# Kernel optimization log

Hardware: AMD Instinct MI355X
Metric: run time of the kernel (lower is better)

Reference implementation:

```python
import jax, jax.numpy as jnp
import numpy as np

N, NFEAT, NHID, NOUT = 16384, 300, 512, 256
NACT, NEIGH, P_EDGE = 64, 2048, 0.002


def setup_inputs() -> dict:
    key = jax.random.key(0)
    ks = jax.random.split(key, 8)
    # Dense KG adjacency (0/1 float), as implied by adj[current_idx][:, current_idx]
    adj = jax.random.bernoulli(ks[0], P_EDGE, (N, N)).astype(jnp.float32)
    x = jax.random.normal(ks[1], (N, NFEAT), dtype=jnp.float32)
    # get_neighbour_nodes(adj, active_idx): nodes adjacent to any active node,
    # excluding the active nodes themselves. Data-dependent size in torch; we
    # compute it exactly here with numpy and fix the length to NEIGH for jit.
    rng = np.random.default_rng(0)
    active = np.sort(rng.choice(N, NACT, replace=False)).astype(np.int64)
    adj_np = np.asarray(adj)
    mask = adj_np[active].sum(0) > 0
    mask[active] = False
    nb = np.nonzero(mask)[0].astype(np.int64)
    nb = np.resize(nb, NEIGH)  # truncate (or wrap-pad) to fixed size
    # GCN + importance-net parameters
    W1 = jax.random.normal(ks[2], (NFEAT, NHID), dtype=jnp.float32) / np.sqrt(NFEAT)
    W2 = jax.random.normal(ks[3], (NHID, NOUT), dtype=jnp.float32) / np.sqrt(NHID)
    imp_w = jax.random.normal(ks[4], (NOUT, 1), dtype=jnp.float32) / np.sqrt(NOUT)
    imp_b = jnp.zeros((1,), dtype=jnp.float32)
    return {"x": x, "adj": adj, "active_idx": jnp.asarray(active),
            "neighbor_idx": jnp.asarray(nb), "W1": W1, "W2": W2,
            "imp_w": imp_w, "imp_b": imp_b}


def reference(x, adj, active_idx, neighbor_idx, W1, W2, imp_w, imp_b):
    # current subgraph = active nodes followed by their neighbors
    cur = jnp.concatenate([active_idx, neighbor_idx])          # [S], S = NACT+NEIGH
    x_sub = x[cur]                                             # [S, nfeat] gather
    a_sub = adj[cur][:, cur]                                   # [S, S] double gather
    # 2-layer GCN (eval mode: dropout inactive): h = A (relu(A (X W1))) W2
    h = jax.nn.relu(a_sub @ (x_sub @ W1))                      # [S, nhid]
    h = a_sub @ (h @ W2)                                       # [S, nout]
    # Importance net: one graph-conv step to a scalar score per node
    imp = ((a_sub @ h) @ imp_w + imp_b)[:, 0]                  # [S]
    # F.normalize(imp, p=1, dim=0)
    imp = imp / jnp.maximum(jnp.sum(jnp.abs(imp)), 1e-12)
    # torch.topk(imp[NACT:], k=3) is computed but unused for the return value
    return imp[NACT:], neighbor_idx
```

## Files before the change

kernel.cpp:

```cpp
#include <hip/hip_runtime.h>

#define NTOT  16384
#define NFEAT 300
#define NHID  512
#define NOUT  256
#define NACT  64
#define NEIGH 2048
#define SSZ   2112
#define CSTR  64
#define GEMMT 528
#define K1BLK (SSZ + GEMMT + 8 + 1)

union SM1 {
    struct { int scur[2304]; unsigned long long smask[9][4]; int spre[40]; } scan;
    struct { float As[16][36]; float Bs[16][64]; } gemm;
};

__global__ __launch_bounds__(256) void k_front(
        const float* __restrict__ adj, const int* __restrict__ act,
        const int* __restrict__ nb,  const float* __restrict__ x,
        const float* __restrict__ W1, const float* __restrict__ W2,
        const float* __restrict__ iw,
        int* __restrict__ cnt, unsigned short* __restrict__ cols,
        float* __restrict__ B1, float* __restrict__ u,
        float* __restrict__ out)
{
    __shared__ SM1 sm;
    const int t = threadIdx.x;
    const int w = t >> 6, lane = t & 63;
    const int bid = blockIdx.x;

    if (bid < SSZ) {
        for (int k = t; k < 2304; k += 256)
            sm.scan.scur[k] = (k < NACT) ? act[k] : (k < SSZ ? nb[k - NACT] : 0);
        __syncthreads();
        const int row = bid;
        const float* arow = adj + (size_t)sm.scan.scur[row] * NTOT;
        float val[9];
#pragma unroll
        for (int k = 0; k < 9; ++k) val[k] = arow[sm.scan.scur[t + (k << 8)]];
        bool hit[9];
#pragma unroll
        for (int k = 0; k < 9; ++k) {
            int j = t + (k << 8);
            hit[k] = (j < SSZ) && (val[k] != 0.0f);
            unsigned long long m = __ballot(hit[k]);
            if (lane == 0) sm.scan.smask[k][w] = m;
        }
        __syncthreads();
        if (t < 64) {
            int c = (t < 36) ? __popcll(sm.scan.smask[t >> 2][t & 3]) : 0;
            int vv = c;
#pragma unroll
            for (int o = 1; o < 64; o <<= 1) {
                int xx = __shfl_up(vv, o, 64);
                if (lane >= o) vv += xx;
            }
            if (t == 0) sm.scan.spre[0] = 0;
            if (t < 36) sm.scan.spre[t + 1] = vv;
        }
        __syncthreads();
        unsigned short* dst = cols + (size_t)row * CSTR;
#pragma unroll
        for (int k = 0; k < 9; ++k) {
            if (hit[k]) {
                unsigned long long below = sm.scan.smask[k][w] & ((1ull << lane) - 1ull);
                dst[sm.scan.spre[k * 4 + w] + __popcll(below)] =
                    (unsigned short)(t + (k << 8));
            }
        }
        if (t == 0) cnt[row] = sm.scan.spre[36];
    } else if (bid < SSZ + GEMMT) {
        int it = bid - SSZ;
        int bm = (it % 66) * 32, bn = (it / 66) * 64;
        int tx = t & 15, ty = t >> 4;
        float acc[2][4] = {};
        for (int kt = 0; kt < NFEAT; kt += 16) {
#pragma unroll
            for (int l = 0; l < 2; ++l) {
                int idx = t + l * 256;
                int m = idx >> 4, kk = idx & 15;
                int gk = kt + kk, gm = bm + m;
                int ar = (gm < NACT) ? act[gm] : nb[gm - NACT];
                sm.gemm.As[kk][m] = (gk < NFEAT) ? x[(size_t)ar * NFEAT + gk] : 0.0f;
            }
#pragma unroll
            for (int l = 0; l < 4; ++l) {
                int idx = t + l * 256;
                int nn = idx & 63, kk = idx >> 6;
                int gk = kt + kk;
                sm.gemm.Bs[kk][nn] = (gk < NFEAT) ? W1[(size_t)gk * NHID + bn + nn] : 0.0f;
            }
            __syncthreads();
#pragma unroll
            for (int kk = 0; kk < 16; ++kk) {
                float a0 = sm.gemm.As[kk][ty * 2], a1 = sm.gemm.As[kk][ty * 2 + 1];
                float4 bv = *(const float4*)&sm.gemm.Bs[kk][tx * 4];
                acc[0][0] += a0 * bv.x; acc[0][1] += a0 * bv.y;
                acc[0][2] += a0 * bv.z; acc[0][3] += a0 * bv.w;
                acc[1][0] += a1 * bv.x; acc[1][1] += a1 * bv.y;
                acc[1][2] += a1 * bv.z; acc[1][3] += a1 * bv.w;
            }
            __syncthreads();
        }
#pragma unroll
        for (int r = 0; r < 2; ++r) {
            int gm = bm + ty * 2 + r;
            *(float4*)&B1[(size_t)gm * NHID + bn + tx * 4] =
                make_float4(acc[r][0], acc[r][1], acc[r][2], acc[r][3]);
        }
    } else if (bid < SSZ + GEMMT + 8) {
        int r0 = (bid - SSZ - GEMMT) * 64;
        for (int r = r0 + w; r < r0 + 64; r += 4) {
            float p = 0.0f;
#pragma unroll
            for (int q = 0; q < 4; ++q)
                p += W2[(size_t)r * NOUT + lane + q * 64] * iw[lane + q * 64];
#pragma unroll
            for (int o = 32; o > 0; o >>= 1) p += __shfl_down(p, o, 64);
            if (lane == 0) u[r] = p;
        }
    } else {
        for (int i = t; i < NEIGH; i += 256) out[NEIGH + i] = (float)nb[i];
    }
}

__global__ __launch_bounds__(256) void k_spmv(const float* __restrict__ B1,
                                              const int* __restrict__ cnt,
                                              const unsigned short* __restrict__ cols,
                                              const float* __restrict__ u,
                                              float* __restrict__ v) {
    __shared__ float su[NHID];
    __shared__ float wsum[4];
    int t = threadIdx.x, row = blockIdx.x;
    su[t] = u[t]; su[t + 256] = u[t + 256];

    int n = cnt[row];
    const unsigned short* cl = cols + (size_t)row * CSTR;
    float a0 = 0.0f, a1 = 0.0f;
    for (int k = 0; k < n; ++k) {
        int j = cl[k];
        a0 += B1[(size_t)j * NHID + t];
        a1 += B1[(size_t)j * NHID + t + 256];
    }
    __syncthreads();
    float p = fmaxf(a0, 0.0f) * su[t] + fmaxf(a1, 0.0f) * su[t + 256];
#pragma unroll
    for (int o = 32; o > 0; o >>= 1) p += __shfl_down(p, o, 64);
    if ((t & 63) == 0) wsum[t >> 6] = p;
    __syncthreads();
    if (t == 0) v[row] = wsum[0] + wsum[1] + wsum[2] + wsum[3];
}

__global__ __launch_bounds__(1024) void k_final(const int* __restrict__ cnt,
                                                const unsigned short* __restrict__ cols,
                                                const float* __restrict__ v,
                                                const float* __restrict__ ib,
                                                float* __restrict__ out) {
    __shared__ float sv[SSZ];
    __shared__ float s1[SSZ];
    __shared__ float s2[SSZ];
    __shared__ int   sc[SSZ];
    __shared__ float wsum[16];
    __shared__ float inv;
    int t = threadIdx.x;
    for (int i = t; i < SSZ; i += 1024) { sv[i] = v[i]; sc[i] = cnt[i]; }
    __syncthreads();
    for (int i = t; i < SSZ; i += 1024) {
        const unsigned short* cl = cols + (size_t)i * CSTR;
        int n = sc[i];
        float s = 0.0f;
        for (int k = 0; k < n; ++k) s += sv[cl[k]];
        s1[i] = s;
    }
    __syncthreads();
    float bias = ib[0];
    for (int i = t; i < SSZ; i += 1024) {
        const unsigned short* cl = cols + (size_t)i * CSTR;
        int n = sc[i];
        float s = 0.0f;
        for (int k = 0; k < n; ++k) s += s1[cl[k]];
        s2[i] = s + bias;
    }
    __syncthreads();
    float s = 0.0f;
    for (int i = t; i < SSZ; i += 1024) s += fabsf(s2[i]);
#pragma unroll
    for (int o = 32; o > 0; o >>= 1) s += __shfl_down(s, o, 64);
    if ((t & 63) == 0) wsum[t >> 6] = s;
    __syncthreads();
    if (t == 0) {
        float tot = 0.0f;
#pragma unroll
        for (int k = 0; k < 16; ++k) tot += wsum[k];
        inv = 1.0f / fmaxf(tot, 1e-12f);
    }
    __syncthreads();
    for (int i = t; i < NEIGH; i += 1024) out[i] = s2[NACT + i] * inv;
}

extern "C" void kernel_launch(void* const* d_in, const int* in_sizes, int n_in,
                              void* d_out, int out_size, void* d_ws, size_t ws_size,
                              hipStream_t stream) {
    const float* x   = (const float*)d_in[0];
    const float* adj = (const float*)d_in[1];
    const int*   act = (const int*)d_in[2];
    const int*   nb  = (const int*)d_in[3];
    const float* W1  = (const float*)d_in[4];
    const float* W2  = (const float*)d_in[5];
    const float* iw  = (const float*)d_in[6];
    const float* ib  = (const float*)d_in[7];
    float* out = (float*)d_out;

    char* ws = (char*)d_ws;
    int*            cnt  = (int*)           (ws + 0);
    unsigned short* cols = (unsigned short*)(ws + 8704);
    float*          B1   = (float*)         (ws + 279040);
    float*          u    = (float*)         (ws + 4604416);
    float*          v    = (float*)         (ws + 4606464);

    k_front<<<dim3(K1BLK), 256,  0, stream>>>(adj, act, nb, x, W1, W2, iw,
                                              cnt, cols, B1, u, out);
    k_spmv <<<dim3(SSZ),   256,  0, stream>>>(B1, cnt, cols, u, v);
    k_final<<<dim3(1),     1024, 0, stream>>>(cnt, cols, v, ib, out);
}
```

Measured before the change: 108.2 us.

## Stream full adjacency rows coalesced and match nonzeros against subgraph indices

Previously, building the subgraph adjacency read 2112 scattered floats from each selected adjacency row, so nearly every load touched a separate cache line. Each block now reads its full 16384-entry row with coalesced float4 loads and compacts the few nonzero column ids into a shared list with a wave prefix scan. It then marks subgraph columns by comparing their node ids against that list. This trades far fewer scattered cache lines for more total bytes read plus a small compare loop. It relies on fixed caps (8 nonzeros per thread, 160 per row) that hold for the sparse test density but would silently drop edges on denser rows.

```diff
diff --git a/kernel.cpp b/kernel.cpp
--- a/kernel.cpp
+++ b/kernel.cpp
@@ -8,11 +8,19 @@
 #define NEIGH 2048
 #define SSZ   2112
 #define CSTR  64
+#define LCAP  160
 #define GEMMT 528
 #define K1BLK (SSZ + GEMMT + 8 + 1)
 
 union SM1 {
-    struct { int scur[2304]; unsigned long long smask[9][4]; int spre[40]; } scan;
+    struct {
+        int scur[2304];
+        unsigned long long smask[9][4];
+        int spre[40];
+        unsigned short L[LCAP];
+        int wtot[4];
+        int snc;
+    } scan;
     struct { float As[16][36]; float Bs[16][64]; } gemm;
 };
 
@@ -31,19 +39,58 @@
     const int bid = blockIdx.x;
 
     if (bid < SSZ) {
+        int rowid = (bid < NACT) ? act[bid] : nb[bid - NACT];
+        const float4* rowv = (const float4*)(adj + (size_t)rowid * NTOT);
+
         for (int k = t; k < 2304; k += 256)
             sm.scan.scur[k] = (k < NACT) ? act[k] : (k < SSZ ? nb[k - NACT] : 0);
-        __syncthreads();
-        const int row = bid;
-        const float* arow = adj + (size_t)sm.scan.scur[row] * NTOT;
-        float val[9];
-#pragma unroll
-        for (int k = 0; k < 9; ++k) val[k] = arow[sm.scan.scur[t + (k << 8)]];
-        bool hit[9];
+
+        unsigned short loc[8];
+        int myc = 0;
+#pragma unroll
+        for (int h = 0; h < 2; ++h) {
+            float4 vv[8];
+#pragma unroll
+            for (int k = 0; k < 8; ++k) vv[k] = rowv[t + ((h * 8 + k) << 8)];
+#pragma unroll
+            for (int k = 0; k < 8; ++k) {
+                int cb = (t + ((h * 8 + k) << 8)) << 2;
+                if (vv[k].x != 0.0f && myc < 8) loc[myc++] = (unsigned short)cb;
+                if (vv[k].y != 0.0f && myc < 8) loc[myc++] = (unsigned short)(cb + 1);
+                if (vv[k].z != 0.0f && myc < 8) loc[myc++] = (unsigned short)(cb + 2);
+                if (vv[k].w != 0.0f && myc < 8) loc[myc++] = (unsigned short)(cb + 3);
+            }
+        }
+        int iv = myc;
+#pragma unroll
+        for (int o = 1; o < 64; o <<= 1) {
+            int xx = __shfl_up(iv, o, 64);
+            if (lane >= o) iv += xx;
+        }
+        if (lane == 63) sm.scan.wtot[w] = iv;
+        __syncthreads();
+        int base = 0;
+        for (int i = 0; i < w; ++i) base += sm.scan.wtot[i];
+        int off = base + iv - myc;
+        for (int i = 0; i < myc; ++i)
+            if (off + i < LCAP) sm.scan.L[off + i] = loc[i];
+        if (t == 255) sm.scan.snc = min(off + myc, LCAP);
+        __syncthreads();
+
+        const int snc = sm.scan.snc;
+        int scurj[9];
+#pragma unroll
+        for (int k = 0; k < 9; ++k) scurj[k] = sm.scan.scur[t + (k << 8)];
+        bool hit[9] = {false,false,false,false,false,false,false,false,false};
+        for (int i = 0; i < snc; ++i) {
+            int ci = sm.scan.L[i];
+#pragma unroll
+            for (int k = 0; k < 9; ++k) hit[k] |= (scurj[k] == ci);
+        }
 #pragma unroll
         for (int k = 0; k < 9; ++k) {
             int j = t + (k << 8);
-            hit[k] = (j < SSZ) && (val[k] != 0.0f);
+            hit[k] = hit[k] && (j < SSZ);
             unsigned long long m = __ballot(hit[k]);
             if (lane == 0) sm.scan.smask[k][w] = m;
         }
@@ -60,7 +107,7 @@
             if (t < 36) sm.scan.spre[t + 1] = vv;
         }
         __syncthreads();
-        unsigned short* dst = cols + (size_t)row * CSTR;
+        unsigned short* dst = cols + (size_t)bid * CSTR;
 #pragma unroll
         for (int k = 0; k < 9; ++k) {
             if (hit[k]) {
@@ -69,7 +116,7 @@
                     (unsigned short)(t + (k << 8));
             }
         }
-        if (t == 0) cnt[row] = sm.scan.spre[36];
+        if (t == 0) cnt[bid] = sm.scan.spre[36];
     } else if (bid < SSZ + GEMMT) {
         int it = bid - SSZ;
         int bm = (it % 66) * 32, bn = (it / 66) * 64;
```

Result: slower. 138.7 us (+28.1%).

## Stream full adjacency rows into shared bitmap instead of scattered column gathers

Applied to the files above, without the earlier changes.

Each adjacency-row block now reads the entire 64KB row with coalesced float4 loads, builds a shared-memory bitmap of nonzeros via atomicOr, and then looks up the 2112 subgraph columns in that bitmap. This replaces 2112 scattered 4-byte loads, each touching a separate cache line. GEMM blocks are also moved to the front of the grid so they are scheduled earlier. The trade-off is more registers per thread (16 float4) and a larger shared footprint, plus shared-memory atomics.

```diff
diff --git a/kernel.cpp b/kernel.cpp
--- a/kernel.cpp
+++ b/kernel.cpp
@@ -9,10 +9,15 @@
 #define SSZ   2112
 #define CSTR  64
 #define GEMMT 528
-#define K1BLK (SSZ + GEMMT + 8 + 1)
+#define K1BLK (GEMMT + SSZ + 8 + 1)
 
 union SM1 {
-    struct { int scur[2304]; unsigned long long smask[9][4]; int spre[40]; } scan;
+    struct {
+        int scur[2304];
+        unsigned int bm[512];
+        unsigned long long smask[9][4];
+        int spre[40];
+    } scan;
     struct { float As[16][36]; float Bs[16][64]; } gemm;
 };
 
@@ -30,49 +35,9 @@
     const int w = t >> 6, lane = t & 63;
     const int bid = blockIdx.x;
 
-    if (bid < SSZ) {
-        for (int k = t; k < 2304; k += 256)
-            sm.scan.scur[k] = (k < NACT) ? act[k] : (k < SSZ ? nb[k - NACT] : 0);
-        __syncthreads();
-        const int row = bid;
-        const float* arow = adj + (size_t)sm.scan.scur[row] * NTOT;
-        float val[9];
-#pragma unroll
-        for (int k = 0; k < 9; ++k) val[k] = arow[sm.scan.scur[t + (k << 8)]];
-        bool hit[9];
-#pragma unroll
-        for (int k = 0; k < 9; ++k) {
-            int j = t + (k << 8);
-            hit[k] = (j < SSZ) && (val[k] != 0.0f);
-            unsigned long long m = __ballot(hit[k]);
-            if (lane == 0) sm.scan.smask[k][w] = m;
-        }
-        __syncthreads();
-        if (t < 64) {
-            int c = (t < 36) ? __popcll(sm.scan.smask[t >> 2][t & 3]) : 0;
-            int vv = c;
-#pragma unroll
-            for (int o = 1; o < 64; o <<= 1) {
-                int xx = __shfl_up(vv, o, 64);
-                if (lane >= o) vv += xx;
-            }
-            if (t == 0) sm.scan.spre[0] = 0;
-            if (t < 36) sm.scan.spre[t + 1] = vv;
-        }
-        __syncthreads();
-        unsigned short* dst = cols + (size_t)row * CSTR;
-#pragma unroll
-        for (int k = 0; k < 9; ++k) {
-            if (hit[k]) {
-                unsigned long long below = sm.scan.smask[k][w] & ((1ull << lane) - 1ull);
-                dst[sm.scan.spre[k * 4 + w] + __popcll(below)] =
-                    (unsigned short)(t + (k << 8));
-            }
-        }
-        if (t == 0) cnt[row] = sm.scan.spre[36];
-    } else if (bid < SSZ + GEMMT) {
-        int it = bid - SSZ;
-        int bm = (it % 66) * 32, bn = (it / 66) * 64;
+    if (bid < GEMMT) {
+        int it = bid;
+        int bm_ = (it % 66) * 32, bn = (it / 66) * 64;
         int tx = t & 15, ty = t >> 4;
         float acc[2][4] = {};
         for (int kt = 0; kt < NFEAT; kt += 16) {
@@ -80,7 +45,7 @@
             for (int l = 0; l < 2; ++l) {
                 int idx = t + l * 256;
                 int m = idx >> 4, kk = idx & 15;
-                int gk = kt + kk, gm = bm + m;
+                int gk = kt + kk, gm = bm_ + m;
                 int ar = (gm < NACT) ? act[gm] : nb[gm - NACT];
                 sm.gemm.As[kk][m] = (gk < NFEAT) ? x[(size_t)ar * NFEAT + gk] : 0.0f;
             }
@@ -105,12 +70,70 @@
         }
 #pragma unroll
         for (int r = 0; r < 2; ++r) {
-            int gm = bm + ty * 2 + r;
+            int gm = bm_ + ty * 2 + r;
             *(float4*)&B1[(size_t)gm * NHID + bn + tx * 4] =
                 make_float4(acc[r][0], acc[r][1], acc[r][2], acc[r][3]);
         }
-    } else if (bid < SSZ + GEMMT + 8) {
-        int r0 = (bid - SSZ - GEMMT) * 64;
+    } else if (bid < GEMMT + SSZ) {
+        const int row = bid - GEMMT;
+        int rowid = (row < NACT) ? act[row] : nb[row - NACT];
+        const float4* rowv = (const float4*)(adj + (size_t)rowid * NTOT);
+
+        float4 vv[16];
+#pragma unroll
+        for (int k = 0; k < 16; ++k) vv[k] = rowv[t + (k << 8)];
+
+        for (int k = t; k < 2304; k += 256)
+            sm.scan.scur[k] = (k < NACT) ? act[k] : (k < SSZ ? nb[k - NACT] : 0);
+        for (int k = t; k < 512; k += 256) sm.scan.bm[k] = 0;
+        __syncthreads();
+
+#pragma unroll
+        for (int k = 0; k < 16; ++k) {
+            int cb = (t + (k << 8)) << 2;
+            unsigned int m = 0;
+            if (vv[k].x != 0.0f) m |= 1u << ((cb + 0) & 31);
+            if (vv[k].y != 0.0f) m |= 1u << ((cb + 1) & 31);
+            if (vv[k].z != 0.0f) m |= 1u << ((cb + 2) & 31);
+            if (vv[k].w != 0.0f) m |= 1u << ((cb + 3) & 31);
+            if (m) atomicOr(&sm.scan.bm[cb >> 5], m);
+        }
+        __syncthreads();
+
+        bool hit[9];
+#pragma unroll
+        for (int k = 0; k < 9; ++k) {
+            int j = t + (k << 8);
+            int c = sm.scan.scur[j];
+            hit[k] = (j < SSZ) && ((sm.scan.bm[c >> 5] >> (c & 31)) & 1u);
+            unsigned long long m = __ballot(hit[k]);
+            if (lane == 0) sm.scan.smask[k][w] = m;
+        }
+        __syncthreads();
+        if (t < 64) {
+            int c = (t < 36) ? __popcll(sm.scan.smask[t >> 2][t & 3]) : 0;
+            int vvp = c;
+#pragma unroll
+            for (int o = 1; o < 64; o <<= 1) {
+                int xx = __shfl_up(vvp, o, 64);
+                if (lane >= o) vvp += xx;
+            }
+            if (t == 0) sm.scan.spre[0] = 0;
+            if (t < 36) sm.scan.spre[t + 1] = vvp;
+        }
+        __syncthreads();
+        unsigned short* dst = cols + (size_t)row * CSTR;
+#pragma unroll
+        for (int k = 0; k < 9; ++k) {
+            if (hit[k]) {
+                unsigned long long below = sm.scan.smask[k][w] & ((1ull << lane) - 1ull);
+                dst[sm.scan.spre[k * 4 + w] + __popcll(below)] =
+                    (unsigned short)(t + (k << 8));
+            }
+        }
+        if (t == 0) cnt[row] = sm.scan.spre[36];
+    } else if (bid < GEMMT + SSZ + 8) {
+        int r0 = (bid - GEMMT - SSZ) * 64;
         for (int r = r0 + w; r < r0 + 64; r += 4) {
             float p = 0.0f;
 #pragma unroll
```

Measured after the change: 97.99 us. -9.5%, faster.
